# Kernel tuning notes

Hardware: AMD Instinct MI355X
Metric: run time of the kernel (lower is better)

The kernel has to match this reference:

```python
import jax, jax.numpy as jnp
import numpy as np

N = 100000  # nodes
E = 1600000  # edges


def _gcn_norm(edge_index, num_nodes):
    # PyG GCNConv default: add self-loops, symmetric normalization.
    src, dst = edge_index[0], edge_index[1]
    loop = jnp.arange(num_nodes, dtype=src.dtype)
    src = jnp.concatenate([src, loop])
    dst = jnp.concatenate([dst, loop])
    deg = jax.ops.segment_sum(jnp.ones_like(dst, dtype=jnp.float32), dst,
                              num_segments=num_nodes)
    dinv = jnp.where(deg > 0, jax.lax.rsqrt(deg), 0.0)
    norm = dinv[src] * dinv[dst]  # [E + N]
    return src, dst, norm


def _gcn_layer(x, W, b, src, dst, norm, num_nodes):
    h = x @ W                                # [N, out]
    msg = h[src] * norm[:, None]             # gather + scale, [E+N, out]
    agg = jax.ops.segment_sum(msg, dst, num_segments=num_nodes)
    return agg + b


def setup_inputs() -> dict:
    key = jax.random.key(0)
    ks = jax.random.split(key, 8)
    d_in, d_h, d_out = 128, 128, 64
    x = jax.random.normal(ks[0], (N, d_in), dtype=jnp.float32)
    edge_index = jax.random.randint(ks[1], (2, E), 0, N, dtype=jnp.int64)
    def glorot(k, fan_in, fan_out):
        s = jnp.sqrt(6.0 / (fan_in + fan_out)).astype(jnp.float32)
        return jax.random.uniform(k, (fan_in, fan_out), jnp.float32, -s, s)
    return {
        "x": x,
        "edge_index": edge_index,
        "W1": glorot(ks[2], d_in, d_h), "b1": jnp.zeros((d_h,), jnp.float32),
        "W2": glorot(ks[3], d_h, d_h), "b2": jnp.zeros((d_h,), jnp.float32),
        "W3": glorot(ks[4], d_h, d_out), "b3": jnp.zeros((d_out,), jnp.float32),
    }


def reference(x, edge_index, W1, b1, W2, b2, W3, b3):
    src, dst, norm = _gcn_norm(edge_index, N)
    h = jax.nn.relu(_gcn_layer(x, W1, b1, src, dst, norm, N))
    h = jax.nn.relu(_gcn_layer(h, W2, b2, src, dst, norm, N))
    h = jax.nn.relu(_gcn_layer(h, W3, b3, src, dst, norm, N))
    return h
```

## Files before the change

### kernel.cpp

```cpp
#include <hip/hip_runtime.h>
#include <hip/hip_bf16.h>
#include <hip/hip_fp16.h>


constexpr int N_NODES = 100000;
constexpr int E_EDGES = 1600000;
constexpr int SCAN_B = (N_NODES + 1023) / 1024;

typedef short short8 __attribute__((ext_vector_type(8)));
typedef float f32x4 __attribute__((ext_vector_type(4)));

__global__ __launch_bounds__(256) void rank_kernel(
    const int* __restrict__ dst, int* __restrict__ cnt,
    int* __restrict__ eRank) {
  int e = blockIdx.x * 256 + threadIdx.x;
  if (e < E_EDGES) eRank[e] = atomicAdd(&cnt[dst[e]], 1);
}

__global__ __launch_bounds__(256) void scan_part_kernel(
    const int* __restrict__ cnt, int* __restrict__ bsum) {
  __shared__ int red[256];
  const int t = threadIdx.x;
  int base = blockIdx.x * 1024 + t * 4;
  int4 v = make_int4(0, 0, 0, 0);
  if (base < N_NODES) v = *(const int4*)(cnt + base);
  red[t] = v.x + v.y + v.z + v.w;
  __syncthreads();
  for (int off = 128; off > 0; off >>= 1) {
    if (t < off) red[t] += red[t + off];
    __syncthreads();
  }
  if (t == 0) bsum[blockIdx.x] = red[0];
}

__global__ __launch_bounds__(128) void scan_tops_kernel(
    const int* __restrict__ bsum, int* __restrict__ boff,
    int* __restrict__ rowptr) {
  __shared__ int part[128];
  const int t = threadIdx.x;
  int v = (t < SCAN_B) ? bsum[t] : 0;
  part[t] = v;
  __syncthreads();
  for (int off = 1; off < 128; off <<= 1) {
    int add = (t >= off) ? part[t - off] : 0;
    __syncthreads();
    part[t] += add;
    __syncthreads();
  }
  if (t < SCAN_B) boff[t] = part[t] - v;
  if (t == 127) rowptr[N_NODES] = part[127];
}

__global__ __launch_bounds__(256) void scan_write_kernel(
    const int* __restrict__ cnt, const int* __restrict__ boff,
    int* __restrict__ rowptr, float* __restrict__ dinv) {
  __shared__ int part[256];
  const int t = threadIdx.x;
  int base = blockIdx.x * 1024 + t * 4;
  int4 v = make_int4(0, 0, 0, 0);
  if (base < N_NODES) v = *(const int4*)(cnt + base);
  int s = v.x + v.y + v.z + v.w;
  part[t] = s;
  __syncthreads();
  for (int off = 1; off < 256; off <<= 1) {
    int add = (t >= off) ? part[t - off] : 0;
    __syncthreads();
    part[t] += add;
    __syncthreads();
  }
  if (base < N_NODES) {
    int run = boff[blockIdx.x] + part[t] - s;
    int4 o;
    o.x = run;
    o.y = run + v.x;
    o.z = run + v.x + v.y;
    o.w = run + v.x + v.y + v.z;
    *(int4*)(rowptr + base) = o;
    float4 dv;
    dv.x = rsqrtf((float)v.x + 1.0f);
    dv.y = rsqrtf((float)v.y + 1.0f);
    dv.z = rsqrtf((float)v.z + 1.0f);
    dv.w = rsqrtf((float)v.w + 1.0f);
    *(float4*)(dinv + base) = dv;
  }
}

__global__ __launch_bounds__(256) void place_kernel(
    const int* __restrict__ src, const int* __restrict__ dst,
    const int* __restrict__ eRank, const int* __restrict__ rowptr,
    const float* __restrict__ dinv, int2* __restrict__ eSW) {
  int e = blockIdx.x * 256 + threadIdx.x;
  if (e < E_EDGES) {
    int d = dst[e];
    int s = src[e];
    int pos = rowptr[d] + eRank[e];
    eSW[pos] = make_int2(s, __float_as_int(dinv[s] * dinv[d]));
  }
}

__device__ inline ushort bf_round(float x) {
  uint u = __float_as_uint(x);
  return (ushort)((u + 0x7FFFu + ((u >> 16) & 1u)) >> 16);
}
__device__ inline ushort bf_split(float x, float* rem) {
  ushort h = bf_round(x);
  *rem = x - __uint_as_float((uint)h << 16);
  return h;
}

template <int OC>
__global__ __launch_bounds__(256) void packw_kernel(
    const float* __restrict__ W, ushort* __restrict__ hi,
    ushort* __restrict__ lo) {
  int id = blockIdx.x * 256 + threadIdx.x;
  if (id >= OC * 16) return;
  int col = id & 15;
  int g = (id >> 4) & 3;
  int ks = (id >> 6) & 3;
  int nt = id >> 8;
  int k0 = ks * 32 + g * 8;
  int n = nt * 16 + col;
  ushort h8[8], l8[8];
#pragma unroll
  for (int j = 0; j < 8; ++j) {
    float rem;
    h8[j] = bf_split(W[(size_t)(k0 + j) * OC + n], &rem);
    l8[j] = bf_round(rem);
  }
  size_t base = (size_t)id * 8;
#pragma unroll
  for (int j = 0; j < 8; ++j) {
    hi[base + j] = h8[j];
    lo[base + j] = l8[j];
  }
}

template <int OC>
__global__ __launch_bounds__(256) void gemm_kernel(
    const float* __restrict__ X, const ushort* __restrict__ Whi,
    const ushort* __restrict__ Wlo, __half* __restrict__ H) {
  constexpr int NT = OC / 16;
  __shared__ ushort sWhi[OC * 128];
  __shared__ ushort sWlo[OC * 128];
  const int t = threadIdx.x;
  {
    const uint4* gh = (const uint4*)Whi;
    const uint4* gl = (const uint4*)Wlo;
    uint4* sh = (uint4*)sWhi;
    uint4* sl = (uint4*)sWlo;
    for (int i = t; i < OC * 128 / 8; i += 256) {
      sh[i] = gh[i];
      sl[i] = gl[i];
    }
  }
  const int wid = t >> 6;
  const int lane = t & 63;
  const int row = blockIdx.x * 64 + wid * 16 + (lane & 15);
  const bool ok = row < N_NODES;
  const int g = lane >> 4;

  short8 ahi[4], alo[4];
  const float* xr = X + (size_t)row * 128;
#pragma unroll
  for (int ks = 0; ks < 4; ++ks) {
    float f[8];
    if (ok) {
      float4 f0 = *(const float4*)(xr + ks * 32 + g * 8);
      float4 f1 = *(const float4*)(xr + ks * 32 + g * 8 + 4);
      f[0] = f0.x; f[1] = f0.y; f[2] = f0.z; f[3] = f0.w;
      f[4] = f1.x; f[5] = f1.y; f[6] = f1.z; f[7] = f1.w;
    } else {
#pragma unroll
      for (int j = 0; j < 8; ++j) f[j] = 0.f;
    }
    union { short8 v; ushort u[8]; } h, l;
#pragma unroll
    for (int j = 0; j < 8; ++j) {
      float rem;
      h.u[j] = bf_split(f[j], &rem);
      l.u[j] = bf_round(rem);
    }
    ahi[ks] = h.v;
    alo[ks] = l.v;
  }
  __syncthreads();

#pragma unroll
  for (int nt = 0; nt < NT; ++nt) {
    f32x4 acc = {0.f, 0.f, 0.f, 0.f};
#pragma unroll
    for (int ks = 0; ks < 4; ++ks) {
      int off = (((nt * 4 + ks) * 4 + g) * 16 + (lane & 15)) * 8;
      short8 bhi = *(const short8*)&sWhi[off];
      short8 blo = *(const short8*)&sWlo[off];
      acc = __builtin_amdgcn_mfma_f32_16x16x32_bf16(alo[ks], bhi, acc, 0, 0, 0);
      acc = __builtin_amdgcn_mfma_f32_16x16x32_bf16(ahi[ks], blo, acc, 0, 0, 0);
      acc = __builtin_amdgcn_mfma_f32_16x16x32_bf16(ahi[ks], bhi, acc, 0, 0, 0);
    }
#pragma unroll
    for (int r = 0; r < 4; ++r) {
      int rr = blockIdx.x * 64 + wid * 16 + g * 4 + r;
      if (rr < N_NODES)
        H[(size_t)rr * OC + nt * 16 + (lane & 15)] = __float2half(acc[r]);
    }
  }
}

template <int OC>
__global__ __launch_bounds__(256) void agg_kernel(
    const __half* __restrict__ H, const int* __restrict__ rowptr,
    const int2* __restrict__ eSW, const float* __restrict__ dinv,
    const float* __restrict__ bias, float* __restrict__ Y) {
  const int wave = threadIdx.x >> 6;
  const int lane = threadIdx.x & 63;
  const int n = blockIdx.x * 4 + wave;
  if (n >= N_NODES) return;
  const float dn = dinv[n];
  const float selfw = dn * dn;
  const int beg = rowptr[n], end = rowptr[n + 1];
  const int jal = min(beg + (beg & 1), end);
  const int jend = jal + ((end - jal) & ~7);
  const int jend2 = jend + ((end - jend) & ~1);

  if constexpr (OC == 128) {
    const __half2* H2 = (const __half2*)H;
    float2 hv = __half22float2(H2[(size_t)n * 64 + lane]);
    float ax = hv.x * selfw, ay = hv.y * selfw;
    for (int j = beg; j < jal; ++j) {
      int2 p = eSW[j];
      float2 v = __half22float2(H2[(size_t)p.x * 64 + lane]);
      float w = __int_as_float(p.y);
      ax = fmaf(v.x, w, ax);
      ay = fmaf(v.y, w, ay);
    }
    for (int j = jal; j < jend; j += 8) {
      int4 p0 = *(const int4*)(eSW + j);
      int4 p1 = *(const int4*)(eSW + j + 2);
      int4 p2 = *(const int4*)(eSW + j + 4);
      int4 p3 = *(const int4*)(eSW + j + 6);
      __half2 h0 = H2[(size_t)p0.x * 64 + lane];
      __half2 h1 = H2[(size_t)p0.z * 64 + lane];
      __half2 h2 = H2[(size_t)p1.x * 64 + lane];
      __half2 h3 = H2[(size_t)p1.z * 64 + lane];
      __half2 h4 = H2[(size_t)p2.x * 64 + lane];
      __half2 h5 = H2[(size_t)p2.z * 64 + lane];
      __half2 h6 = H2[(size_t)p3.x * 64 + lane];
      __half2 h7 = H2[(size_t)p3.z * 64 + lane];
      float2 v0 = __half22float2(h0);
      float2 v1 = __half22float2(h1);
      float2 v2 = __half22float2(h2);
      float2 v3 = __half22float2(h3);
      float2 v4 = __half22float2(h4);
      float2 v5 = __half22float2(h5);
      float2 v6 = __half22float2(h6);
      float2 v7 = __half22float2(h7);
      ax = fmaf(v0.x, __int_as_float(p0.y), ax);
      ay = fmaf(v0.y, __int_as_float(p0.y), ay);
      ax = fmaf(v1.x, __int_as_float(p0.w), ax);
      ay = fmaf(v1.y, __int_as_float(p0.w), ay);
      ax = fmaf(v2.x, __int_as_float(p1.y), ax);
      ay = fmaf(v2.y, __int_as_float(p1.y), ay);
      ax = fmaf(v3.x, __int_as_float(p1.w), ax);
      ay = fmaf(v3.y, __int_as_float(p1.w), ay);
      ax = fmaf(v4.x, __int_as_float(p2.y), ax);
      ay = fmaf(v4.y, __int_as_float(p2.y), ay);
      ax = fmaf(v5.x, __int_as_float(p2.w), ax);
      ay = fmaf(v5.y, __int_as_float(p2.w), ay);
      ax = fmaf(v6.x, __int_as_float(p3.y), ax);
      ay = fmaf(v6.y, __int_as_float(p3.y), ay);
      ax = fmaf(v7.x, __int_as_float(p3.w), ax);
      ay = fmaf(v7.y, __int_as_float(p3.w), ay);
    }
    for (int j = jend; j < jend2; j += 2) {
      int4 p = *(const int4*)(eSW + j);
      float2 v0 = __half22float2(H2[(size_t)p.x * 64 + lane]);
      float2 v1 = __half22float2(H2[(size_t)p.z * 64 + lane]);
      ax = fmaf(v0.x, __int_as_float(p.y), ax);
      ay = fmaf(v0.y, __int_as_float(p.y), ay);
      ax = fmaf(v1.x, __int_as_float(p.w), ax);
      ay = fmaf(v1.y, __int_as_float(p.w), ay);
    }
    for (int j = jend2; j < end; ++j) {
      int2 p = eSW[j];
      float2 v = __half22float2(H2[(size_t)p.x * 64 + lane]);
      float w = __int_as_float(p.y);
      ax = fmaf(v.x, w, ax);
      ay = fmaf(v.y, w, ay);
    }
    float2 bb = ((const float2*)bias)[lane];
    float2 o;
    o.x = fmaxf(ax + bb.x, 0.f);
    o.y = fmaxf(ay + bb.y, 0.f);
    ((float2*)Y)[(size_t)n * 64 + lane] = o;
  } else {
    float a = __half2float(H[(size_t)n * 64 + lane]) * selfw;
    for (int j = beg; j < jal; ++j) {
      int2 p = eSW[j];
      a = fmaf(__half2float(H[(size_t)p.x * 64 + lane]),
               __int_as_float(p.y), a);
    }
    for (int j = jal; j < jend; j += 8) {
      int4 p0 = *(const int4*)(eSW + j);
      int4 p1 = *(const int4*)(eSW + j + 2);
      int4 p2 = *(const int4*)(eSW + j + 4);
      int4 p3 = *(const int4*)(eSW + j + 6);
      __half h0 = H[(size_t)p0.x * 64 + lane];
      __half h1 = H[(size_t)p0.z * 64 + lane];
      __half h2 = H[(size_t)p1.x * 64 + lane];
      __half h3 = H[(size_t)p1.z * 64 + lane];
      __half h4 = H[(size_t)p2.x * 64 + lane];
      __half h5 = H[(size_t)p2.z * 64 + lane];
      __half h6 = H[(size_t)p3.x * 64 + lane];
      __half h7 = H[(size_t)p3.z * 64 + lane];
      a = fmaf(__half2float(h0), __int_as_float(p0.y), a);
      a = fmaf(__half2float(h1), __int_as_float(p0.w), a);
      a = fmaf(__half2float(h2), __int_as_float(p1.y), a);
      a = fmaf(__half2float(h3), __int_as_float(p1.w), a);
      a = fmaf(__half2float(h4), __int_as_float(p2.y), a);
      a = fmaf(__half2float(h5), __int_as_float(p2.w), a);
      a = fmaf(__half2float(h6), __int_as_float(p3.y), a);
      a = fmaf(__half2float(h7), __int_as_float(p3.w), a);
    }
    for (int j = jend; j < jend2; j += 2) {
      int4 p = *(const int4*)(eSW + j);
      a = fmaf(__half2float(H[(size_t)p.x * 64 + lane]),
               __int_as_float(p.y), a);
      a = fmaf(__half2float(H[(size_t)p.z * 64 + lane]),
               __int_as_float(p.w), a);
    }
    for (int j = jend2; j < end; ++j) {
      int2 p = eSW[j];
      a = fmaf(__half2float(H[(size_t)p.x * 64 + lane]),
               __int_as_float(p.y), a);
    }
    Y[(size_t)n * 64 + lane] = fmaxf(a + bias[lane], 0.f);
  }
}

extern "C" void kernel_launch(void* const* d_in, const int* in_sizes, int n_in,
                              void* d_out, int out_size, void* d_ws,
                              size_t ws_size, hipStream_t stream) {
  const float* x = (const float*)d_in[0];
  const int* ei = (const int*)d_in[1];
  const float* W1 = (const float*)d_in[2];
  const float* b1 = (const float*)d_in[3];
  const float* W2 = (const float*)d_in[4];
  const float* b2 = (const float*)d_in[5];
  const float* W3 = (const float*)d_in[6];
  const float* b3 = (const float*)d_in[7];
  const int* src = ei;
  const int* dst = ei + E_EDGES;

  size_t off = 0;
  auto alloc = [&](size_t bytes) -> void* {
    void* p = (char*)d_ws + off;
    off += (bytes + 255) & ~(size_t)255;
    return p;
  };
  int* cnt = (int*)alloc((size_t)N_NODES * 4);
  int* rowptr = (int*)alloc((size_t)(N_NODES + 1) * 4);
  float* dinv = (float*)alloc((size_t)N_NODES * 4);
  int* bsum = (int*)alloc((size_t)SCAN_B * 4);
  int* boff = (int*)alloc((size_t)SCAN_B * 4);
  int* eRank = (int*)alloc((size_t)E_EDGES * 4);
  int2* eSW = (int2*)alloc((size_t)E_EDGES * 8);
  __half* h = (__half*)alloc((size_t)N_NODES * 128 * 2);
  float* A = (float*)alloc((size_t)N_NODES * 128 * 4);
  ushort* wp1h = (ushort*)alloc((size_t)128 * 128 * 2);
  ushort* wp1l = (ushort*)alloc((size_t)128 * 128 * 2);
  ushort* wp2h = (ushort*)alloc((size_t)128 * 128 * 2);
  ushort* wp2l = (ushort*)alloc((size_t)128 * 128 * 2);
  ushort* wp3h = (ushort*)alloc((size_t)128 * 64 * 2);
  ushort* wp3l = (ushort*)alloc((size_t)128 * 64 * 2);

  hipMemsetAsync(cnt, 0, (size_t)N_NODES * 4, stream);

  const int EB = (E_EDGES + 255) / 256;
  rank_kernel<<<EB, 256, 0, stream>>>(dst, cnt, eRank);
  scan_part_kernel<<<SCAN_B, 256, 0, stream>>>(cnt, bsum);
  scan_tops_kernel<<<1, 128, 0, stream>>>(bsum, boff, rowptr);
  scan_write_kernel<<<SCAN_B, 256, 0, stream>>>(cnt, boff, rowptr, dinv);
  place_kernel<<<EB, 256, 0, stream>>>(src, dst, eRank, rowptr, dinv, eSW);
  packw_kernel<128><<<8, 256, 0, stream>>>(W1, wp1h, wp1l);
  packw_kernel<128><<<8, 256, 0, stream>>>(W2, wp2h, wp2l);
  packw_kernel<64><<<4, 256, 0, stream>>>(W3, wp3h, wp3l);

  const int GB = (N_NODES + 63) / 64;
  const int AB = (N_NODES + 3) / 4;

  gemm_kernel<128><<<GB, 256, 0, stream>>>(x, wp1h, wp1l, h);
  agg_kernel<128><<<AB, 256, 0, stream>>>(h, rowptr, eSW, dinv, b1, A);
  gemm_kernel<128><<<GB, 256, 0, stream>>>(A, wp2h, wp2l, h);
  agg_kernel<128><<<AB, 256, 0, stream>>>(h, rowptr, eSW, dinv, b2, A);
  gemm_kernel<64><<<GB, 256, 0, stream>>>(A, wp3h, wp3l, h);
  agg_kernel<64><<<AB, 256, 0, stream>>>(h, rowptr, eSW, dinv, b3,
                                         (float*)d_out);
}
```

Measured before the change: 380.0 us.

## Slice features into 16-wide column blocks and store intermediates as fp16

The GEMM output and the aggregation input/output move to a sliced layout of [slice][node][16 halves], so each aggregation wave handles one 16-feature slice of one node. The wave splits its edges across 8 groups and combines them with shuffles. The intermediate activations between layers are stored as fp16 instead of fp32, and the next GEMM reads them directly. The aim is to keep gathered slices cache-friendly and to cut activation traffic, at the cost of more waves, per-slice re-reading of the edge list, and an extra fp16 rounding of activations.

```diff
diff --git a/kernel.cpp b/kernel.cpp
--- a/kernel.cpp
+++ b/kernel.cpp
@@ -135,9 +135,9 @@
   }
 }
 
-template <int OC>
+template <int OC, bool HALF_IN>
 __global__ __launch_bounds__(256) void gemm_kernel(
-    const float* __restrict__ X, const ushort* __restrict__ Whi,
+    const void* __restrict__ Xv, const ushort* __restrict__ Whi,
     const ushort* __restrict__ Wlo, __half* __restrict__ H) {
   constexpr int NT = OC / 16;
   __shared__ ushort sWhi[OC * 128];
@@ -160,15 +160,28 @@
   const int g = lane >> 4;
 
   short8 ahi[4], alo[4];
-  const float* xr = X + (size_t)row * 128;
 #pragma unroll
   for (int ks = 0; ks < 4; ++ks) {
     float f[8];
     if (ok) {
-      float4 f0 = *(const float4*)(xr + ks * 32 + g * 8);
-      float4 f1 = *(const float4*)(xr + ks * 32 + g * 8 + 4);
-      f[0] = f0.x; f[1] = f0.y; f[2] = f0.z; f[3] = f0.w;
-      f[4] = f1.x; f[5] = f1.y; f[6] = f1.z; f[7] = f1.w;
+      if constexpr (HALF_IN) {
+        int k0 = ks * 32 + g * 8;
+        const __half* Xh = (const __half*)Xv;
+        uint4 u = *(const uint4*)(Xh +
+            ((size_t)(k0 >> 4) * N_NODES + row) * 16 + (k0 & 15));
+        float2 t0 = __half22float2(*(__half2*)&u.x);
+        float2 t1 = __half22float2(*(__half2*)&u.y);
+        float2 t2 = __half22float2(*(__half2*)&u.z);
+        float2 t3 = __half22float2(*(__half2*)&u.w);
+        f[0] = t0.x; f[1] = t0.y; f[2] = t1.x; f[3] = t1.y;
+        f[4] = t2.x; f[5] = t2.y; f[6] = t3.x; f[7] = t3.y;
+      } else {
+        const float* xr = (const float*)Xv + (size_t)row * 128;
+        float4 f0 = *(const float4*)(xr + ks * 32 + g * 8);
+        float4 f1 = *(const float4*)(xr + ks * 32 + g * 8 + 4);
+        f[0] = f0.x; f[1] = f0.y; f[2] = f0.z; f[3] = f0.w;
+        f[4] = f1.x; f[5] = f1.y; f[6] = f1.z; f[7] = f1.w;
+      }
     } else {
 #pragma unroll
       for (int j = 0; j < 8; ++j) f[j] = 0.f;
@@ -201,139 +214,64 @@
     for (int r = 0; r < 4; ++r) {
       int rr = blockIdx.x * 64 + wid * 16 + g * 4 + r;
       if (rr < N_NODES)
-        H[(size_t)rr * OC + nt * 16 + (lane & 15)] = __float2half(acc[r]);
-    }
-  }
-}
-
-template <int OC>
+        H[((size_t)nt * N_NODES + rr) * 16 + (lane & 15)] =
+            __float2half(acc[r]);
+    }
+  }
+}
+
+template <int NSLICE, bool FINAL>
 __global__ __launch_bounds__(256) void agg_kernel(
     const __half* __restrict__ H, const int* __restrict__ rowptr,
     const int2* __restrict__ eSW, const float* __restrict__ dinv,
-    const float* __restrict__ bias, float* __restrict__ Y) {
+    const float* __restrict__ bias, void* __restrict__ out) {
   const int wave = threadIdx.x >> 6;
   const int lane = threadIdx.x & 63;
-  const int n = blockIdx.x * 4 + wave;
-  if (n >= N_NODES) return;
+  const int unit = blockIdx.x * 4 + wave;
+  const int slice = unit / N_NODES;
+  const int n = unit - slice * N_NODES;
+  const int g = lane >> 3;
+  const int f = lane & 7;
   const float dn = dinv[n];
+  const int beg = rowptr[n], end = rowptr[n + 1];
+  const __half2* Hs = (const __half2*)H + (size_t)slice * N_NODES * 8;
+
+  float ax = 0.f, ay = 0.f;
+  int j = beg + g;
+  for (; j + 8 < end; j += 16) {
+    int2 p0 = eSW[j];
+    int2 p1 = eSW[j + 8];
+    float2 v0 = __half22float2(Hs[(size_t)p0.x * 8 + f]);
+    float2 v1 = __half22float2(Hs[(size_t)p1.x * 8 + f]);
+    float w0 = __int_as_float(p0.y);
+    float w1 = __int_as_float(p1.y);
+    ax = fmaf(v0.x, w0, ax); ay = fmaf(v0.y, w0, ay);
+    ax = fmaf(v1.x, w1, ax); ay = fmaf(v1.y, w1, ay);
+  }
+  if (j < end) {
+    int2 p = eSW[j];
+    float2 v = __half22float2(Hs[(size_t)p.x * 8 + f]);
+    float w = __int_as_float(p.y);
+    ax = fmaf(v.x, w, ax); ay = fmaf(v.y, w, ay);
+  }
+  ax += __shfl_xor(ax, 8);  ay += __shfl_xor(ay, 8);
+  ax += __shfl_xor(ax, 16); ay += __shfl_xor(ay, 16);
+  ax += __shfl_xor(ax, 32); ay += __shfl_xor(ay, 32);
+  float2 sv = __half22float2(Hs[(size_t)n * 8 + f]);
   const float selfw = dn * dn;
-  const int beg = rowptr[n], end = rowptr[n + 1];
-  const int jal = min(beg + (beg & 1), end);
-  const int jend = jal + ((end - jal) & ~7);
-  const int jend2 = jend + ((end - jend) & ~1);
-
-  if constexpr (OC == 128) {
-    const __half2* H2 = (const __half2*)H;
-    float2 hv = __half22float2(H2[(size_t)n * 64 + lane]);
-    float ax = hv.x * selfw, ay = hv.y * selfw;
-    for (int j = beg; j < jal; ++j) {
-      int2 p = eSW[j];
-      float2 v = __half22float2(H2[(size_t)p.x * 64 + lane]);
-      float w = __int_as_float(p.y);
-      ax = fmaf(v.x, w, ax);
-      ay = fmaf(v.y, w, ay);
-    }
-    for (int j = jal; j < jend; j += 8) {
-      int4 p0 = *(const int4*)(eSW + j);
-      int4 p1 = *(const int4*)(eSW + j + 2);
-      int4 p2 = *(const int4*)(eSW + j + 4);
-      int4 p3 = *(const int4*)(eSW + j + 6);
-      __half2 h0 = H2[(size_t)p0.x * 64 + lane];
-      __half2 h1 = H2[(size_t)p0.z * 64 + lane];
-      __half2 h2 = H2[(size_t)p1.x * 64 + lane];
-      __half2 h3 = H2[(size_t)p1.z * 64 + lane];
-      __half2 h4 = H2[(size_t)p2.x * 64 + lane];
-      __half2 h5 = H2[(size_t)p2.z * 64 + lane];
-      __half2 h6 = H2[(size_t)p3.x * 64 + lane];
-      __half2 h7 = H2[(size_t)p3.z * 64 + lane];
-      float2 v0 = __half22float2(h0);
-      float2 v1 = __half22float2(h1);
-      float2 v2 = __half22float2(h2);
-      float2 v3 = __half22float2(h3);
-      float2 v4 = __half22float2(h4);
-      float2 v5 = __half22float2(h5);
-      float2 v6 = __half22float2(h6);
-      float2 v7 = __half22float2(h7);
-      ax = fmaf(v0.x, __int_as_float(p0.y), ax);
-      ay = fmaf(v0.y, __int_as_float(p0.y), ay);
-      ax = fmaf(v1.x, __int_as_float(p0.w), ax);
-      ay = fmaf(v1.y, __int_as_float(p0.w), ay);
-      ax = fmaf(v2.x, __int_as_float(p1.y), ax);
-      ay = fmaf(v2.y, __int_as_float(p1.y), ay);
-      ax = fmaf(v3.x, __int_as_float(p1.w), ax);
-      ay = fmaf(v3.y, __int_as_float(p1.w), ay);
-      ax = fmaf(v4.x, __int_as_float(p2.y), ax);
-      ay = fmaf(v4.y, __int_as_float(p2.y), ay);
-      ax = fmaf(v5.x, __int_as_float(p2.w), ax);
-      ay = fmaf(v5.y, __int_as_float(p2.w), ay);
-      ax = fmaf(v6.x, __int_as_float(p3.y), ax);
-      ay = fmaf(v6.y, __int_as_float(p3.y), ay);
-      ax = fmaf(v7.x, __int_as_float(p3.w), ax);
-      ay = fmaf(v7.y, __int_as_float(p3.w), ay);
-    }
-    for (int j = jend; j < jend2; j += 2) {
-      int4 p = *(const int4*)(eSW + j);
-      float2 v0 = __half22float2(H2[(size_t)p.x * 64 + lane]);
-      float2 v1 = __half22float2(H2[(size_t)p.z * 64 + lane]);
-      ax = fmaf(v0.x, __int_as_float(p.y), ax);
-      ay = fmaf(v0.y, __int_as_float(p.y), ay);
-      ax = fmaf(v1.x, __int_as_float(p.w), ax);
-      ay = fmaf(v1.y, __int_as_float(p.w), ay);
-    }
-    for (int j = jend2; j < end; ++j) {
-      int2 p = eSW[j];
-      float2 v = __half22float2(H2[(size_t)p.x * 64 + lane]);
-      float w = __int_as_float(p.y);
-      ax = fmaf(v.x, w, ax);
-      ay = fmaf(v.y, w, ay);
-    }
-    float2 bb = ((const float2*)bias)[lane];
-    float2 o;
-    o.x = fmaxf(ax + bb.x, 0.f);
-    o.y = fmaxf(ay + bb.y, 0.f);
-    ((float2*)Y)[(size_t)n * 64 + lane] = o;
-  } else {
-    float a = __half2float(H[(size_t)n * 64 + lane]) * selfw;
-    for (int j = beg; j < jal; ++j) {
-      int2 p = eSW[j];
-      a = fmaf(__half2float(H[(size_t)p.x * 64 + lane]),
-               __int_as_float(p.y), a);
-    }
-    for (int j = jal; j < jend; j += 8) {
-      int4 p0 = *(const int4*)(eSW + j);
-      int4 p1 = *(const int4*)(eSW + j + 2);
-      int4 p2 = *(const int4*)(eSW + j + 4);
-      int4 p3 = *(const int4*)(eSW + j + 6);
-      __half h0 = H[(size_t)p0.x * 64 + lane];
-      __half h1 = H[(size_t)p0.z * 64 + lane];
-      __half h2 = H[(size_t)p1.x * 64 + lane];
-      __half h3 = H[(size_t)p1.z * 64 + lane];
-      __half h4 = H[(size_t)p2.x * 64 + lane];
-      __half h5 = H[(size_t)p2.z * 64 + lane];
-      __half h6 = H[(size_t)p3.x * 64 + lane];
-      __half h7 = H[(size_t)p3.z * 64 + lane];
-      a = fmaf(__half2float(h0), __int_as_float(p0.y), a);
-      a = fmaf(__half2float(h1), __int_as_float(p0.w), a);
-      a = fmaf(__half2float(h2), __int_as_float(p1.y), a);
-      a = fmaf(__half2float(h3), __int_as_float(p1.w), a);
-      a = fmaf(__half2float(h4), __int_as_float(p2.y), a);
-      a = fmaf(__half2float(h5), __int_as_float(p2.w), a);
-      a = fmaf(__half2float(h6), __int_as_float(p3.y), a);
-      a = fmaf(__half2float(h7), __int_as_float(p3.w), a);
-    }
-    for (int j = jend; j < jend2; j += 2) {
-      int4 p = *(const int4*)(eSW + j);
-      a = fmaf(__half2float(H[(size_t)p.x * 64 + lane]),
-               __int_as_float(p.y), a);
-      a = fmaf(__half2float(H[(size_t)p.z * 64 + lane]),
-               __int_as_float(p.w), a);
-    }
-    for (int j = jend2; j < end; ++j) {
-      int2 p = eSW[j];
-      a = fmaf(__half2float(H[(size_t)p.x * 64 + lane]),
-               __int_as_float(p.y), a);
-    }
-    Y[(size_t)n * 64 + lane] = fmaxf(a + bias[lane], 0.f);
+  ax = fmaf(sv.x, selfw, ax);
+  ay = fmaf(sv.y, selfw, ay);
+  float2 bb = *(const float2*)(bias + slice * 16 + 2 * f);
+  ax = fmaxf(ax + bb.x, 0.f);
+  ay = fmaxf(ay + bb.y, 0.f);
+  if (g == 0) {
+    if constexpr (FINAL) {
+      *(float2*)((float*)out + (size_t)n * 64 + slice * 16 + 2 * f) =
+          make_float2(ax, ay);
+    } else {
+      ((__half2*)out)[((size_t)slice * N_NODES + n) * 8 + f] =
+          __floats2half2_rn(ax, ay);
+    }
   }
 }
 
@@ -365,7 +303,7 @@
   int* eRank = (int*)alloc((size_t)E_EDGES * 4);
   int2* eSW = (int2*)alloc((size_t)E_EDGES * 8);
   __half* h = (__half*)alloc((size_t)N_NODES * 128 * 2);
-  float* A = (float*)alloc((size_t)N_NODES * 128 * 4);
+  __half* A = (__half*)alloc((size_t)N_NODES * 128 * 2);
   ushort* wp1h = (ushort*)alloc((size_t)128 * 128 * 2);
   ushort* wp1l = (ushort*)alloc((size_t)128 * 128 * 2);
   ushort* wp2h = (ushort*)alloc((size_t)128 * 128 * 2);
@@ -386,13 +324,14 @@
   packw_kernel<64><<<4, 256, 0, stream>>>(W3, wp3h, wp3l);
 
   const int GB = (N_NODES + 63) / 64;
-  const int AB = (N_NODES + 3) / 4;
-
-  gemm_kernel<128><<<GB, 256, 0, stream>>>(x, wp1h, wp1l, h);
-  agg_kernel<128><<<AB, 256, 0, stream>>>(h, rowptr, eSW, dinv, b1, A);
-  gemm_kernel<128><<<GB, 256, 0, stream>>>(A, wp2h, wp2l, h);
-  agg_kernel<128><<<AB, 256, 0, stream>>>(h, rowptr, eSW, dinv, b2, A);
-  gemm_kernel<64><<<GB, 256, 0, stream>>>(A, wp3h, wp3l, h);
-  agg_kernel<64><<<AB, 256, 0, stream>>>(h, rowptr, eSW, dinv, b3,
-                                         (float*)d_out);
-}
+  const int AB128 = 8 * N_NODES / 4;
+  const int AB64 = 4 * N_NODES / 4;
+
+  gemm_kernel<128, false><<<GB, 256, 0, stream>>>(x, wp1h, wp1l, h);
+  agg_kernel<8, false><<<AB128, 256, 0, stream>>>(h, rowptr, eSW, dinv, b1, A);
+  gemm_kernel<128, true><<<GB, 256, 0, stream>>>(A, wp2h, wp2l, h);
+  agg_kernel<8, false><<<AB128, 256, 0, stream>>>(h, rowptr, eSW, dinv, b2, A);
+  gemm_kernel<64, true><<<GB, 256, 0, stream>>>(A, wp3h, wp3l, h);
+  agg_kernel<4, true><<<AB64, 256, 0, stream>>>(h, rowptr, eSW, dinv, b3,
+                                                d_out);
+}
```

Result: slower. 791.8 us (+108.4%).
